# Kernel tuning notes

Measured on AMD Instinct MI355X. Metric: run time of the kernel, lower is better.

The kernel has to match this reference:

```python
import jax, jax.numpy as jnp
import numpy as np
from jax import lax

B = 512
MBD_B, MBD_C = 64, 16
FEAT = 40 * 4 * 4  # 640


def _conv(x, w, b):
    y = lax.conv_general_dilated(x, w, (1, 1), 'VALID',
                                 dimension_numbers=('NCHW', 'OIHW', 'NCHW'))
    return y + b[None, :, None, None]


def _maxpool2(x):
    return lax.reduce_window(x, -jnp.inf, lax.max,
                             (1, 1, 2, 2), (1, 1, 2, 2), 'VALID')


def setup_inputs() -> dict:
    key = jax.random.key(0)
    ks = jax.random.split(key, 10)
    def he(k, shape, fan_in):
        return jax.random.normal(k, shape, dtype=jnp.float32) * np.float32(1.0 / np.sqrt(fan_in))
    return {
        'x': jax.random.normal(ks[0], (B, 1, 28, 28), dtype=jnp.float32),
        'conv1_w': he(ks[1], (20, 1, 5, 5), 25),
        'conv1_b': jnp.zeros((20,), jnp.float32),
        'conv2_w': he(ks[2], (40, 20, 5, 5), 20 * 25),
        'conv2_b': jnp.zeros((40,), jnp.float32),
        'T': he(ks[3], (MBD_B * MBD_C, FEAT), FEAT),          # feature_scan_tensor (no bias)
        'fc1_w': he(ks[4], (100, FEAT + MBD_B), FEAT + MBD_B),
        'fc1_b': jnp.zeros((100,), jnp.float32),
        'fc2_w': he(ks[5], (1, 100), 100),
        'fc2_b': jnp.zeros((1,), jnp.float32),
    }


def reference(x, conv1_w, conv1_b, conv2_w, conv2_b, T, fc1_w, fc1_b, fc2_w, fc2_b):
    # conv feature extractor: [B,1,28,28] -> [B,40,4,4]
    h = _maxpool2(jax.nn.relu(_conv(x, conv1_w, conv1_b)))
    h = _maxpool2(jax.nn.relu(_conv(h, conv2_w, conv2_b)))
    feats = h.reshape(h.shape[0], -1)  # [B, 640]

    # minibatch discrimination: M = feats @ T^T -> [B, b, c]
    M = (feats @ T.T).reshape(-1, MBD_B, MBD_C)
    # pairwise L1 over c: [B, B, b] (includes j==i diagonal = 0, exp(0)=1, as in original)
    dist = jnp.abs(M[:, None, :, :] - M[None, :, :, :]).sum(axis=3)
    closeness = jnp.exp(-dist).sum(axis=1)  # [B, b]

    out = jnp.concatenate([feats, closeness], axis=1)  # [B, 640+b]
    out = jax.nn.relu(out @ fc1_w.T + fc1_b)
    # Dropout(p=0.2) omitted (deterministic eval-mode reference)
    out = jax.nn.sigmoid(out @ fc2_w.T + fc2_b)  # [B, 1]
    return out
```

## Files before the change

kernel.cpp:

```cpp
#include <hip/hip_runtime.h>


__global__ __launch_bounds__(256) void k0_wxform(const float* __restrict__ w,
                                                 float* __restrict__ ws) {
  const int e = blockIdx.x * 256 + threadIdx.x;
  if (e >= 32000) return;
  const int ocHalf = e / 16000;
  const int r = e - ocHalf * 16000;
  const int ic = r / 800;
  const int r2 = r - ic * 800;
  const int tap = r2 >> 5;
  const int slot = r2 & 31;
  const int q = slot & 7;
  const int grp = slot >> 3;
  float val = 0.f;
  if (q < 5) val = w[(ocHalf * 20 + grp * 5 + q) * 500 + ic * 25 + tap];
  ws[e] = val;
}

__global__ __launch_bounds__(128) void k1_conv1_pool(
    const float* __restrict__ x, const float* __restrict__ w,
    const float* __restrict__ bias, float* __restrict__ out) {
  __shared__ __align__(16) float img[784];
  __shared__ float wl[250];
  __shared__ float bl[10];
  const int imgId = blockIdx.x >> 1;
  const int half = blockIdx.x & 1;
  {
    const float4* src = reinterpret_cast<const float4*>(x + imgId * 784);
    float4* dst = reinterpret_cast<float4*>(img);
    for (int t = threadIdx.x; t < 196; t += 128) dst[t] = src[t];
  }
  for (int t = threadIdx.x; t < 250; t += 128) wl[t] = w[half * 250 + t];
  if (threadIdx.x < 10) bl[threadIdx.x] = bias[half * 10 + threadIdx.x];
  __syncthreads();

  for (int o = threadIdx.x; o < 1440; o += 128) {
    const int chl = o / 144;
    const int rem = o - chl * 144;
    const int py = rem / 12;
    const int px = rem - py * 12;
    const int oy = py * 2, ox = px * 2;
    float p[6][6];
    const float* ib = &img[oy * 28 + ox];
#pragma unroll
    for (int r = 0; r < 6; ++r) {
      const float2 v0 = *reinterpret_cast<const float2*>(&ib[r * 28 + 0]);
      const float2 v1 = *reinterpret_cast<const float2*>(&ib[r * 28 + 2]);
      const float2 v2 = *reinterpret_cast<const float2*>(&ib[r * 28 + 4]);
      p[r][0] = v0.x; p[r][1] = v0.y; p[r][2] = v1.x;
      p[r][3] = v1.y; p[r][4] = v2.x; p[r][5] = v2.y;
    }
    const float* wc = &wl[chl * 25];
    float s00 = 0.f, s01 = 0.f, s10 = 0.f, s11 = 0.f;
#pragma unroll
    for (int ky = 0; ky < 5; ++ky) {
#pragma unroll
      for (int kx = 0; kx < 5; ++kx) {
        const float ww = wc[ky * 5 + kx];
        s00 += p[ky][kx] * ww;
        s01 += p[ky][kx + 1] * ww;
        s10 += p[ky + 1][kx] * ww;
        s11 += p[ky + 1][kx + 1] * ww;
      }
    }
    const float m = fmaxf(fmaxf(s00, s01), fmaxf(s10, s11)) + bl[chl];
    out[imgId * 2880 + half * 1440 + o] = fmaxf(m, 0.f);
  }
}

__global__ __launch_bounds__(128) void k2_conv2_pool(
    const float* __restrict__ h1, const float* __restrict__ wsx,
    const float* __restrict__ bias, float* __restrict__ feats) {
  __shared__ __align__(16) float in[2880];
  __shared__ __align__(16) float wl[2][2][25][32];
  __shared__ float part[64][21];
  const int imgId = blockIdx.x >> 1;
  const int half = blockIdx.x & 1;
  const int tid = threadIdx.x;
  const int h = tid >> 6;
  const int grp = (tid >> 4) & 3;
  const int pos = tid & 15;
  const int py = pos >> 2, px = pos & 3;
  const int oy = py * 2, ox = px * 2;

  {
    const float4* src = reinterpret_cast<const float4*>(h1 + imgId * 2880);
    float4* dst = reinterpret_cast<float4*>(in);
    for (int t = tid; t < 720; t += 128) dst[t] = src[t];
  }
  const float4* wsrc = reinterpret_cast<const float4*>(wsx) + half * 4000;
  float4* wdst = reinterpret_cast<float4*>(wl);
  {
#pragma unroll
    for (int k = 0; k < 4; ++k) {
      const int e = tid + k * 128;
      if (e < 400) {
        const int hs = (e >= 200) ? 1 : 0;
        const int idx = e - hs * 200;
        wdst[hs * 400 + idx] = wsrc[(hs * 10 + 0) * 200 + idx];
      }
    }
  }
  __syncthreads();

  float acc[5][4];
#pragma unroll
  for (int q = 0; q < 5; ++q)
#pragma unroll
    for (int pp = 0; pp < 4; ++pp) acc[q][pp] = 0.f;

  for (int s = 0; s < 10; ++s) {
    const int p0 = s & 1;
    float4 sv[4];
    if (s < 9) {
#pragma unroll
      for (int k = 0; k < 4; ++k) {
        const int e = tid + k * 128;
        if (e < 400) {
          const int hs = (e >= 200) ? 1 : 0;
          const int idx = e - hs * 200;
          sv[k] = wsrc[(hs * 10 + s + 1) * 200 + idx];
        }
      }
    }
    const int myic = h * 10 + s;
    float p[6][6];
    {
      const float* ib = &in[myic * 144 + oy * 12 + ox];
#pragma unroll
      for (int r = 0; r < 6; ++r) {
        const float2 v0 = *reinterpret_cast<const float2*>(&ib[r * 12 + 0]);
        const float2 v1 = *reinterpret_cast<const float2*>(&ib[r * 12 + 2]);
        const float2 v2 = *reinterpret_cast<const float2*>(&ib[r * 12 + 4]);
        p[r][0] = v0.x; p[r][1] = v0.y; p[r][2] = v1.x;
        p[r][3] = v1.y; p[r][4] = v2.x; p[r][5] = v2.y;
      }
    }
#pragma unroll
    for (int ky = 0; ky < 5; ++ky) {
#pragma unroll
      for (int kx = 0; kx < 5; ++kx) {
        const int tap = ky * 5 + kx;
        const float4 w4 =
            *reinterpret_cast<const float4*>(&wl[h][p0][tap][grp * 8]);
        const float w4b = wl[h][p0][tap][grp * 8 + 4];
        const float i00 = p[ky][kx];
        const float i01 = p[ky][kx + 1];
        const float i10 = p[ky + 1][kx];
        const float i11 = p[ky + 1][kx + 1];
        acc[0][0] += i00 * w4.x; acc[0][1] += i01 * w4.x;
        acc[0][2] += i10 * w4.x; acc[0][3] += i11 * w4.x;
        acc[1][0] += i00 * w4.y; acc[1][1] += i01 * w4.y;
        acc[1][2] += i10 * w4.y; acc[1][3] += i11 * w4.y;
        acc[2][0] += i00 * w4.z; acc[2][1] += i01 * w4.z;
        acc[2][2] += i10 * w4.z; acc[2][3] += i11 * w4.z;
        acc[3][0] += i00 * w4.w; acc[3][1] += i01 * w4.w;
        acc[3][2] += i10 * w4.w; acc[3][3] += i11 * w4.w;
        acc[4][0] += i00 * w4b; acc[4][1] += i01 * w4b;
        acc[4][2] += i10 * w4b; acc[4][3] += i11 * w4b;
      }
    }
    if (s < 9) {
#pragma unroll
      for (int k = 0; k < 4; ++k) {
        const int e = tid + k * 128;
        if (e < 400) {
          const int hs = (e >= 200) ? 1 : 0;
          const int idx = e - hs * 200;
          wdst[hs * 400 + ((s + 1) & 1) * 200 + idx] = sv[k];
        }
      }
    }
    __syncthreads();
  }

  if (tid >= 64) {
    const int t2 = tid - 64;
#pragma unroll
    for (int q = 0; q < 5; ++q)
#pragma unroll
      for (int pp = 0; pp < 4; ++pp) part[t2][q * 4 + pp] = acc[q][pp];
  }
  __syncthreads();
  if (tid < 64) {
#pragma unroll
    for (int q = 0; q < 5; ++q) {
      const int ch = half * 20 + grp * 5 + q;
      const float a0 = acc[q][0] + part[tid][q * 4 + 0];
      const float a1 = acc[q][1] + part[tid][q * 4 + 1];
      const float a2 = acc[q][2] + part[tid][q * 4 + 2];
      const float a3 = acc[q][3] + part[tid][q * 4 + 3];
      const float m = fmaxf(fmaxf(a0, a1), fmaxf(a2, a3)) + bias[ch];
      feats[imgId * 640 + ch * 16 + pos] = fmaxf(m, 0.f);
    }
  }
}

__global__ __launch_bounds__(128) void k3_gemm(
    const float* __restrict__ A, const float* __restrict__ Bm,
    float* __restrict__ C) {
  __shared__ __align__(16) float As[16][36];
  __shared__ __align__(16) float Bs[16][36];
  const int tid = threadIdx.x;
  const int tx = tid & 15;
  const int ty = tid >> 4;
  const int i0 = blockIdx.y * 16;
  const int j0 = blockIdx.x * 32;
  float acc[2][2] = {{0.f, 0.f}, {0.f, 0.f}};

  for (int k0 = 0; k0 < 640; k0 += 16) {
    if (tid < 64) {
      const int m = tid >> 2, kq = tid & 3;
      const float4 av =
          *reinterpret_cast<const float4*>(A + (i0 + m) * 640 + k0 + kq * 4);
      As[kq * 4 + 0][m] = av.x;
      As[kq * 4 + 1][m] = av.y;
      As[kq * 4 + 2][m] = av.z;
      As[kq * 4 + 3][m] = av.w;
    }
    {
      const int n = tid >> 2, kq = tid & 3;
      const float4 bv =
          *reinterpret_cast<const float4*>(Bm + (j0 + n) * 640 + k0 + kq * 4);
      Bs[kq * 4 + 0][n] = bv.x;
      Bs[kq * 4 + 1][n] = bv.y;
      Bs[kq * 4 + 2][n] = bv.z;
      Bs[kq * 4 + 3][n] = bv.w;
    }
    __syncthreads();
#pragma unroll
    for (int kk = 0; kk < 16; ++kk) {
      const float2 a2 = *reinterpret_cast<const float2*>(&As[kk][ty * 2]);
      const float2 b2 = *reinterpret_cast<const float2*>(&Bs[kk][tx * 2]);
      acc[0][0] += a2.x * b2.x; acc[0][1] += a2.x * b2.y;
      acc[1][0] += a2.y * b2.x; acc[1][1] += a2.y * b2.y;
    }
    __syncthreads();
  }
#pragma unroll
  for (int u = 0; u < 2; ++u) {
    float2 st = make_float2(acc[u][0], acc[u][1]);
    *reinterpret_cast<float2*>(&C[(i0 + ty * 2 + u) * 1024 + j0 + tx * 2]) = st;
  }
}

__global__ __launch_bounds__(256) void k4_mbd(const float* __restrict__ M,
                                              float* __restrict__ cp) {
  __shared__ float4 jb4[2][4][256];
  const int bid = blockIdx.x;
  const int ig = bid >> 4;
  const int jq = bid & 15;
  const int t = threadIdx.x;
  const int b = t & 63;
  const int g = t >> 6;
  const int i0 = ig * 16 + g * 4;
  const float4* Mf4 = reinterpret_cast<const float4*>(M);

  float4 mi[4][4];
#pragma unroll
  for (int u = 0; u < 4; ++u) {
#pragma unroll
    for (int q = 0; q < 4; ++q) mi[u][q] = Mf4[(i0 + u) * 256 + b * 4 + q];
  }
  const int wslot = (t >> 2) * 4 + ((t & 3) ^ ((t >> 3) & 3));
  {
#pragma unroll
    for (int k = 0; k < 4; ++k)
      jb4[0][k][wslot] = Mf4[(jq * 32 + k) * 256 + t];
  }
  __syncthreads();

  float acc[4] = {0.f, 0.f, 0.f, 0.f};
  const int xr = (b >> 1) & 3;
  for (int c = 0; c < 8; ++c) {
    float4 st[4];
    if (c < 7) {
#pragma unroll
      for (int k = 0; k < 4; ++k)
        st[k] = Mf4[(jq * 32 + (c + 1) * 4 + k) * 256 + t];
    }
    const int cbuf = c & 1;
#pragma unroll
    for (int jj = 0; jj < 4; ++jj) {
      const float4* row = jb4[cbuf][jj];
      float4 mj[4];
#pragma unroll
      for (int q = 0; q < 4; ++q) mj[q] = row[b * 4 + (q ^ xr)];
#pragma unroll
      for (int u = 0; u < 4; ++u) {
        float dist =
            fabsf(mi[u][0].x - mj[0].x) + fabsf(mi[u][0].y - mj[0].y) +
            fabsf(mi[u][0].z - mj[0].z) + fabsf(mi[u][0].w - mj[0].w) +
            fabsf(mi[u][1].x - mj[1].x) + fabsf(mi[u][1].y - mj[1].y) +
            fabsf(mi[u][1].z - mj[1].z) + fabsf(mi[u][1].w - mj[1].w) +
            fabsf(mi[u][2].x - mj[2].x) + fabsf(mi[u][2].y - mj[2].y) +
            fabsf(mi[u][2].z - mj[2].z) + fabsf(mi[u][2].w - mj[2].w) +
            fabsf(mi[u][3].x - mj[3].x) + fabsf(mi[u][3].y - mj[3].y) +
            fabsf(mi[u][3].z - mj[3].z) + fabsf(mi[u][3].w - mj[3].w);
        acc[u] += __expf(-dist);
      }
    }
    if (c < 7) {
#pragma unroll
      for (int k = 0; k < 4; ++k) jb4[(c + 1) & 1][k][wslot] = st[k];
    }
    __syncthreads();
  }
#pragma unroll
  for (int u = 0; u < 4; ++u)
    cp[(jq * 512 + i0 + u) * 64 + b] = acc[u];
}

__global__ __launch_bounds__(256) void k5_head(
    const float* __restrict__ feats, const float* __restrict__ cp,
    const float* __restrict__ w1, const float* __restrict__ b1,
    const float* __restrict__ w2, const float* __restrict__ b2,
    float* __restrict__ out) {
  __shared__ __align__(16) float v[704];
  __shared__ float hb[100];
  const int i = blockIdx.x;
  const int tid = threadIdx.x;
  float4* v4 = reinterpret_cast<float4*>(v);
  if (tid < 160)
    v4[tid] = reinterpret_cast<const float4*>(feats + i * 640)[tid];
  if (tid >= 192) {
    const int bb = tid - 192;
    float s = 0.f;
#pragma unroll
    for (int q = 0; q < 16; ++q) s += cp[(q * 512 + i) * 64 + bb];
    v[640 + bb] = s;
  }
  __syncthreads();
  const int wave = tid >> 6;
  const int lane = tid & 63;
  for (int r = wave; r < 100; r += 4) {
    const float4* wr = reinterpret_cast<const float4*>(w1 + r * 704);
    const float4 wa = wr[lane];
    const float4 wb = wr[lane + 64];
    const float4 va = v4[lane];
    const float4 vb = v4[lane + 64];
    float s = wa.x * va.x + wa.y * va.y + wa.z * va.z + wa.w * va.w +
              wb.x * vb.x + wb.y * vb.y + wb.z * vb.z + wb.w * vb.w;
    if (lane < 48) {
      const float4 wc = wr[lane + 128];
      const float4 vc = v4[lane + 128];
      s += wc.x * vc.x + wc.y * vc.y + wc.z * vc.z + wc.w * vc.w;
    }
#pragma unroll
    for (int off = 32; off; off >>= 1) s += __shfl_xor(s, off);
    if (lane == 0) hb[r] = fmaxf(s + b1[r], 0.f) * w2[r];
  }
  __syncthreads();
  if (tid < 64) {
    float s = hb[tid] + ((tid < 36) ? hb[tid + 64] : 0.f);
#pragma unroll
    for (int off = 32; off; off >>= 1) s += __shfl_xor(s, off);
    if (tid == 0) out[i] = 1.f / (1.f + __expf(-(s + b2[0])));
  }
}

extern "C" void kernel_launch(void* const* d_in, const int* in_sizes, int n_in,
                              void* d_out, int out_size, void* d_ws,
                              size_t ws_size, hipStream_t stream) {
  const float* x   = (const float*)d_in[0];
  const float* c1w = (const float*)d_in[1];
  const float* c1b = (const float*)d_in[2];
  const float* c2w = (const float*)d_in[3];
  const float* c2b = (const float*)d_in[4];
  const float* T   = (const float*)d_in[5];
  const float* f1w = (const float*)d_in[6];
  const float* f1b = (const float*)d_in[7];
  const float* f2w = (const float*)d_in[8];
  const float* f2b = (const float*)d_in[9];
  float* out = (float*)d_out;

  float* h1     = (float*)d_ws;
  float* feats  = h1 + 512 * 2880;
  float* M      = feats + 512 * 640;
  float* wstage = M;
  float* cp     = h1;

  k0_wxform<<<125, 256, 0, stream>>>(c2w, wstage);
  k1_conv1_pool<<<1024, 128, 0, stream>>>(x, c1w, c1b, h1);
  k2_conv2_pool<<<1024, 128, 0, stream>>>(h1, wstage, c2b, feats);
  k3_gemm<<<dim3(32, 32), 128, 0, stream>>>(feats, T, M);
  k4_mbd<<<512, 256, 0, stream>>>(M, cp);
  k5_head<<<512, 256, 0, stream>>>(feats, cp, f1w, f1b, f2w, f2b, out);
}
```

Baseline: 195.4 us.

## Fuse conv stages into one kernel and use split-bf16 MFMA for the feature GEMM

Merges conv1+pool and conv2+pool into a single kernel that keeps the first-stage activations in shared memory, handling two images per block. This removes the global round-trip of the intermediate activations and one launch. It also replaces the scalar fp32 GEMM with an MFMA bf16 GEMM that splits each operand into high and low bf16 parts (three products) to approximate fp32 accuracy. The prep kernel now also converts T to hi/lo bf16 every call, which adds extra memory traffic and a small loss of precision in exchange.

```diff
diff --git a/kernel.cpp b/kernel.cpp
--- a/kernel.cpp
+++ b/kernel.cpp
@@ -1,247 +1,301 @@
 #include <hip/hip_runtime.h>
 
 
-__global__ __launch_bounds__(256) void k0_wxform(const float* __restrict__ w,
-                                                 float* __restrict__ ws) {
-  const int e = blockIdx.x * 256 + threadIdx.x;
-  if (e >= 32000) return;
-  const int ocHalf = e / 16000;
-  const int r = e - ocHalf * 16000;
-  const int ic = r / 800;
-  const int r2 = r - ic * 800;
-  const int tap = r2 >> 5;
-  const int slot = r2 & 31;
-  const int q = slot & 7;
-  const int grp = slot >> 3;
-  float val = 0.f;
-  if (q < 5) val = w[(ocHalf * 20 + grp * 5 + q) * 500 + ic * 25 + tap];
-  ws[e] = val;
-}
-
-__global__ __launch_bounds__(128) void k1_conv1_pool(
-    const float* __restrict__ x, const float* __restrict__ w,
-    const float* __restrict__ bias, float* __restrict__ out) {
-  __shared__ __align__(16) float img[784];
-  __shared__ float wl[250];
-  __shared__ float bl[10];
-  const int imgId = blockIdx.x >> 1;
-  const int half = blockIdx.x & 1;
+typedef __attribute__((ext_vector_type(8))) short bf16x8;
+typedef __attribute__((ext_vector_type(4))) float f32x4;
+
+static __device__ __forceinline__ unsigned short f2bf(float x) {
+  unsigned int u = __float_as_uint(x);
+  unsigned int r = (u + 0x7fffu + ((u >> 16) & 1u)) >> 16;
+  return (unsigned short)r;
+}
+static __device__ __forceinline__ float bf2f(unsigned short h) {
+  return __uint_as_float(((unsigned int)h) << 16);
+}
+
+__global__ __launch_bounds__(256) void kP_prep(
+    const float* __restrict__ c2w, const float* __restrict__ T,
+    float* __restrict__ ws2, unsigned short* __restrict__ Th,
+    unsigned short* __restrict__ Tl) {
+  const int idx = blockIdx.x * 256 + threadIdx.x;
+  if (idx < 655360) {
+    const float v = T[idx];
+    const unsigned short h = f2bf(v);
+    Th[idx] = h;
+    Tl[idx] = f2bf(v - bf2f(h));
+  }
+  if (idx < 32000) {
+    const int ic = idx / 1600;
+    const int r = idx - ic * 1600;
+    const int tap = r >> 6;
+    const int slot = r & 63;
+    const int grp = slot >> 3;
+    const int q = slot & 7;
+    float val = 0.f;
+    if (q < 5) val = c2w[(grp * 5 + q) * 500 + ic * 25 + tap];
+    ws2[idx] = val;
+  }
+}
+
+__global__ __launch_bounds__(256) void kC_conv(
+    const float* __restrict__ x, const float* __restrict__ c1w,
+    const float* __restrict__ c1b, const float* __restrict__ ws2,
+    const float* __restrict__ c2b, float* __restrict__ feats,
+    unsigned short* __restrict__ fh, unsigned short* __restrict__ fl) {
+  __shared__ __align__(16) float img[2][784];
+  __shared__ __align__(16) float h1s[2][2880];
+  __shared__ float wl1[500];
+  __shared__ float bl1[20];
+  __shared__ float bl2[40];
+  __shared__ __align__(16) float wl2[2][2][1600];
+  __shared__ float mg[2][64][41];
+
+  const int tid = threadIdx.x;
+  const int slot = tid >> 7;
+  const int lt = tid & 127;
+  const int imgId = blockIdx.x * 2 + slot;
+
   {
-    const float4* src = reinterpret_cast<const float4*>(x + imgId * 784);
-    float4* dst = reinterpret_cast<float4*>(img);
-    for (int t = threadIdx.x; t < 196; t += 128) dst[t] = src[t];
-  }
-  for (int t = threadIdx.x; t < 250; t += 128) wl[t] = w[half * 250 + t];
-  if (threadIdx.x < 10) bl[threadIdx.x] = bias[half * 10 + threadIdx.x];
-  __syncthreads();
-
-  for (int o = threadIdx.x; o < 1440; o += 128) {
-    const int chl = o / 144;
-    const int rem = o - chl * 144;
-    const int py = rem / 12;
-    const int px = rem - py * 12;
-    const int oy = py * 2, ox = px * 2;
-    float p[6][6];
-    const float* ib = &img[oy * 28 + ox];
+    float4* dst = reinterpret_cast<float4*>(&img[0][0]);
+    for (int t = tid; t < 392; t += 256) {
+      const int which = t / 196;
+      const int within = t - which * 196;
+      dst[t] = reinterpret_cast<const float4*>(
+          x + (blockIdx.x * 2 + which) * 784)[within];
+    }
+  }
+  for (int t = tid; t < 500; t += 256) wl1[t] = c1w[t];
+  if (tid < 20) bl1[tid] = c1b[tid];
+  if (tid >= 64 && tid < 104) bl2[tid - 64] = c2b[tid - 64];
+  __syncthreads();
+
+  for (int qd = lt; qd < 720; qd += 128) {
+    const int ch = qd / 36;
+    const int rem = qd - ch * 36;
+    const int py = rem / 3;
+    const int qx = rem - py * 3;
+    const int r0 = py * 2;
+    const int c0 = qx * 8;
+    float p[6][12];
 #pragma unroll
     for (int r = 0; r < 6; ++r) {
-      const float2 v0 = *reinterpret_cast<const float2*>(&ib[r * 28 + 0]);
-      const float2 v1 = *reinterpret_cast<const float2*>(&ib[r * 28 + 2]);
-      const float2 v2 = *reinterpret_cast<const float2*>(&ib[r * 28 + 4]);
-      p[r][0] = v0.x; p[r][1] = v0.y; p[r][2] = v1.x;
-      p[r][3] = v1.y; p[r][4] = v2.x; p[r][5] = v2.y;
-    }
-    const float* wc = &wl[chl * 25];
-    float s00 = 0.f, s01 = 0.f, s10 = 0.f, s11 = 0.f;
+      const float* ib = &img[slot][(r0 + r) * 28 + c0];
+      const float4 a = *reinterpret_cast<const float4*>(ib);
+      const float4 b = *reinterpret_cast<const float4*>(ib + 4);
+      const float4 c = *reinterpret_cast<const float4*>(ib + 8);
+      p[r][0] = a.x; p[r][1] = a.y; p[r][2] = a.z; p[r][3] = a.w;
+      p[r][4] = b.x; p[r][5] = b.y; p[r][6] = b.z; p[r][7] = b.w;
+      p[r][8] = c.x; p[r][9] = c.y; p[r][10] = c.z; p[r][11] = c.w;
+    }
+    float s[16];
+#pragma unroll
+    for (int u = 0; u < 16; ++u) s[u] = 0.f;
+    const float* wc = &wl1[ch * 25];
 #pragma unroll
     for (int ky = 0; ky < 5; ++ky) {
 #pragma unroll
       for (int kx = 0; kx < 5; ++kx) {
-        const float ww = wc[ky * 5 + kx];
-        s00 += p[ky][kx] * ww;
-        s01 += p[ky][kx + 1] * ww;
-        s10 += p[ky + 1][kx] * ww;
-        s11 += p[ky + 1][kx + 1] * ww;
-      }
-    }
-    const float m = fmaxf(fmaxf(s00, s01), fmaxf(s10, s11)) + bl[chl];
-    out[imgId * 2880 + half * 1440 + o] = fmaxf(m, 0.f);
-  }
-}
-
-__global__ __launch_bounds__(128) void k2_conv2_pool(
-    const float* __restrict__ h1, const float* __restrict__ wsx,
-    const float* __restrict__ bias, float* __restrict__ feats) {
-  __shared__ __align__(16) float in[2880];
-  __shared__ __align__(16) float wl[2][2][25][32];
-  __shared__ float part[64][21];
-  const int imgId = blockIdx.x >> 1;
-  const int half = blockIdx.x & 1;
-  const int tid = threadIdx.x;
-  const int h = tid >> 6;
-  const int grp = (tid >> 4) & 3;
-  const int pos = tid & 15;
-  const int py = pos >> 2, px = pos & 3;
-  const int oy = py * 2, ox = px * 2;
+        const float w = wc[ky * 5 + kx];
+#pragma unroll
+        for (int u = 0; u < 4; ++u) {
+#pragma unroll
+          for (int dy = 0; dy < 2; ++dy) {
+#pragma unroll
+            for (int dx = 0; dx < 2; ++dx) {
+              s[u * 4 + dy * 2 + dx] += p[ky + dy][2 * u + dx + kx] * w;
+            }
+          }
+        }
+      }
+    }
+    const float bb = bl1[ch];
+    float4 o;
+    o.x = fmaxf(fmaxf(fmaxf(s[0], s[1]), fmaxf(s[2], s[3])) + bb, 0.f);
+    o.y = fmaxf(fmaxf(fmaxf(s[4], s[5]), fmaxf(s[6], s[7])) + bb, 0.f);
+    o.z = fmaxf(fmaxf(fmaxf(s[8], s[9]), fmaxf(s[10], s[11])) + bb, 0.f);
+    o.w = fmaxf(fmaxf(fmaxf(s[12], s[13]), fmaxf(s[14], s[15])) + bb, 0.f);
+    *reinterpret_cast<float4*>(&h1s[slot][ch * 144 + py * 12 + qx * 4]) = o;
+  }
 
   {
-    const float4* src = reinterpret_cast<const float4*>(h1 + imgId * 2880);
-    float4* dst = reinterpret_cast<float4*>(in);
-    for (int t = tid; t < 720; t += 128) dst[t] = src[t];
-  }
-  const float4* wsrc = reinterpret_cast<const float4*>(wsx) + half * 4000;
-  float4* wdst = reinterpret_cast<float4*>(wl);
-  {
+    float4* wlf4 = reinterpret_cast<float4*>(&wl2[0][0][0]);
+    const float4* wsf4 = reinterpret_cast<const float4*>(ws2);
 #pragma unroll
     for (int k = 0; k < 4; ++k) {
-      const int e = tid + k * 128;
-      if (e < 400) {
-        const int hs = (e >= 200) ? 1 : 0;
-        const int idx = e - hs * 200;
-        wdst[hs * 400 + idx] = wsrc[(hs * 10 + 0) * 200 + idx];
-      }
-    }
-  }
-  __syncthreads();
-
-  float acc[5][4];
+      const int e = tid + k * 256;
+      if (e < 800) {
+        const int str = e / 400;
+        const int i4 = e - str * 400;
+        wlf4[(str * 2 + 0) * 400 + i4] = wsf4[(str * 10 + 0) * 400 + i4];
+      }
+    }
+  }
+  __syncthreads();
+
+  const int h = lt >> 6;
+  const int grp = (lt >> 3) & 7;
+  const int pp = lt & 7;
+  const int oy = (pp >> 1) * 2;
+  const int ox = (pp & 1) * 4;
+  float acc[5][8];
 #pragma unroll
   for (int q = 0; q < 5; ++q)
 #pragma unroll
-    for (int pp = 0; pp < 4; ++pp) acc[q][pp] = 0.f;
-
+    for (int u = 0; u < 8; ++u) acc[q][u] = 0.f;
+
+  float4* wlf4 = reinterpret_cast<float4*>(&wl2[0][0][0]);
+  const float4* wsf4 = reinterpret_cast<const float4*>(ws2);
   for (int s = 0; s < 10; ++s) {
     const int p0 = s & 1;
     float4 sv[4];
     if (s < 9) {
 #pragma unroll
       for (int k = 0; k < 4; ++k) {
-        const int e = tid + k * 128;
-        if (e < 400) {
-          const int hs = (e >= 200) ? 1 : 0;
-          const int idx = e - hs * 200;
-          sv[k] = wsrc[(hs * 10 + s + 1) * 200 + idx];
+        const int e = tid + k * 256;
+        if (e < 800) {
+          const int str = e / 400;
+          const int i4 = e - str * 400;
+          sv[k] = wsf4[(str * 10 + s + 1) * 400 + i4];
         }
       }
     }
-    const int myic = h * 10 + s;
-    float p[6][6];
-    {
-      const float* ib = &in[myic * 144 + oy * 12 + ox];
-#pragma unroll
-      for (int r = 0; r < 6; ++r) {
-        const float2 v0 = *reinterpret_cast<const float2*>(&ib[r * 12 + 0]);
-        const float2 v1 = *reinterpret_cast<const float2*>(&ib[r * 12 + 2]);
-        const float2 v2 = *reinterpret_cast<const float2*>(&ib[r * 12 + 4]);
-        p[r][0] = v0.x; p[r][1] = v0.y; p[r][2] = v1.x;
-        p[r][3] = v1.y; p[r][4] = v2.x; p[r][5] = v2.y;
-      }
-    }
+    const int ic = h * 10 + s;
+    float p[6][8];
+#pragma unroll
+    for (int r = 0; r < 6; ++r) {
+      const float* ib = &h1s[slot][ic * 144 + (oy + r) * 12 + ox];
+      const float4 a = *reinterpret_cast<const float4*>(ib);
+      const float4 b = *reinterpret_cast<const float4*>(ib + 4);
+      p[r][0] = a.x; p[r][1] = a.y; p[r][2] = a.z; p[r][3] = a.w;
+      p[r][4] = b.x; p[r][5] = b.y; p[r][6] = b.z; p[r][7] = b.w;
+    }
+    const float* wbase = &wl2[h][p0][0];
 #pragma unroll
     for (int ky = 0; ky < 5; ++ky) {
 #pragma unroll
       for (int kx = 0; kx < 5; ++kx) {
         const int tap = ky * 5 + kx;
         const float4 w4 =
-            *reinterpret_cast<const float4*>(&wl[h][p0][tap][grp * 8]);
-        const float w4b = wl[h][p0][tap][grp * 8 + 4];
-        const float i00 = p[ky][kx];
-        const float i01 = p[ky][kx + 1];
-        const float i10 = p[ky + 1][kx];
-        const float i11 = p[ky + 1][kx + 1];
-        acc[0][0] += i00 * w4.x; acc[0][1] += i01 * w4.x;
-        acc[0][2] += i10 * w4.x; acc[0][3] += i11 * w4.x;
-        acc[1][0] += i00 * w4.y; acc[1][1] += i01 * w4.y;
-        acc[1][2] += i10 * w4.y; acc[1][3] += i11 * w4.y;
-        acc[2][0] += i00 * w4.z; acc[2][1] += i01 * w4.z;
-        acc[2][2] += i10 * w4.z; acc[2][3] += i11 * w4.z;
-        acc[3][0] += i00 * w4.w; acc[3][1] += i01 * w4.w;
-        acc[3][2] += i10 * w4.w; acc[3][3] += i11 * w4.w;
-        acc[4][0] += i00 * w4b; acc[4][1] += i01 * w4b;
-        acc[4][2] += i10 * w4b; acc[4][3] += i11 * w4b;
+            *reinterpret_cast<const float4*>(&wbase[tap * 64 + grp * 8]);
+        const float w4b = wbase[tap * 64 + grp * 8 + 4];
+#pragma unroll
+        for (int pooled = 0; pooled < 2; ++pooled) {
+#pragma unroll
+          for (int dy = 0; dy < 2; ++dy) {
+#pragma unroll
+            for (int dx = 0; dx < 2; ++dx) {
+              const int u = pooled * 4 + dy * 2 + dx;
+              const float iv = p[ky + dy][pooled * 2 + dx + kx];
+              acc[0][u] += iv * w4.x;
+              acc[1][u] += iv * w4.y;
+              acc[2][u] += iv * w4.z;
+              acc[3][u] += iv * w4.w;
+              acc[4][u] += iv * w4b;
+            }
+          }
+        }
       }
     }
     if (s < 9) {
 #pragma unroll
       for (int k = 0; k < 4; ++k) {
-        const int e = tid + k * 128;
-        if (e < 400) {
-          const int hs = (e >= 200) ? 1 : 0;
-          const int idx = e - hs * 200;
-          wdst[hs * 400 + ((s + 1) & 1) * 200 + idx] = sv[k];
+        const int e = tid + k * 256;
+        if (e < 800) {
+          const int str = e / 400;
+          const int i4 = e - str * 400;
+          wlf4[(str * 2 + ((s + 1) & 1)) * 400 + i4] = sv[k];
         }
       }
     }
     __syncthreads();
   }
 
-  if (tid >= 64) {
-    const int t2 = tid - 64;
+  const int midx = (grp << 3) | pp;
+  if (h == 1) {
 #pragma unroll
     for (int q = 0; q < 5; ++q)
 #pragma unroll
-      for (int pp = 0; pp < 4; ++pp) part[t2][q * 4 + pp] = acc[q][pp];
-  }
-  __syncthreads();
-  if (tid < 64) {
+      for (int u = 0; u < 8; ++u) mg[slot][midx][q * 8 + u] = acc[q][u];
+  }
+  __syncthreads();
+  if (h == 0) {
+    const int pos0 = (pp >> 1) * 4 + (pp & 1) * 2;
 #pragma unroll
     for (int q = 0; q < 5; ++q) {
-      const int ch = half * 20 + grp * 5 + q;
-      const float a0 = acc[q][0] + part[tid][q * 4 + 0];
-      const float a1 = acc[q][1] + part[tid][q * 4 + 1];
-      const float a2 = acc[q][2] + part[tid][q * 4 + 2];
-      const float a3 = acc[q][3] + part[tid][q * 4 + 3];
-      const float m = fmaxf(fmaxf(a0, a1), fmaxf(a2, a3)) + bias[ch];
-      feats[imgId * 640 + ch * 16 + pos] = fmaxf(m, 0.f);
-    }
-  }
-}
-
-__global__ __launch_bounds__(128) void k3_gemm(
-    const float* __restrict__ A, const float* __restrict__ Bm,
-    float* __restrict__ C) {
-  __shared__ __align__(16) float As[16][36];
-  __shared__ __align__(16) float Bs[16][36];
+      const int ch = grp * 5 + q;
+      float a[8];
+#pragma unroll
+      for (int u = 0; u < 8; ++u) a[u] = acc[q][u] + mg[slot][midx][q * 8 + u];
+      const float bb = bl2[ch];
+      const float r0v =
+          fmaxf(fmaxf(fmaxf(a[0], a[1]), fmaxf(a[2], a[3])) + bb, 0.f);
+      const float r1v =
+          fmaxf(fmaxf(fmaxf(a[4], a[5]), fmaxf(a[6], a[7])) + bb, 0.f);
+      const int off = imgId * 640 + ch * 16 + pos0;
+      *reinterpret_cast<float2*>(&feats[off]) = make_float2(r0v, r1v);
+      const unsigned short h0 = f2bf(r0v), h1v = f2bf(r1v);
+      ushort2 hv; hv.x = h0; hv.y = h1v;
+      ushort2 lv;
+      lv.x = f2bf(r0v - bf2f(h0));
+      lv.y = f2bf(r1v - bf2f(h1v));
+      *reinterpret_cast<ushort2*>(&fh[off]) = hv;
+      *reinterpret_cast<ushort2*>(&fl[off]) = lv;
+    }
+  }
+}
+
+__global__ __launch_bounds__(256) void k3m_gemm(
+    const unsigned short* __restrict__ fh, const unsigned short* __restrict__ fl,
+    const unsigned short* __restrict__ Th, const unsigned short* __restrict__ Tl,
+    float* __restrict__ M) {
+  __shared__ short Ah[64][40];
+  __shared__ short Al[64][40];
+  __shared__ short Bh[64][40];
+  __shared__ short Bl[64][40];
   const int tid = threadIdx.x;
-  const int tx = tid & 15;
-  const int ty = tid >> 4;
-  const int i0 = blockIdx.y * 16;
-  const int j0 = blockIdx.x * 32;
-  float acc[2][2] = {{0.f, 0.f}, {0.f, 0.f}};
-
-  for (int k0 = 0; k0 < 640; k0 += 16) {
-    if (tid < 64) {
-      const int m = tid >> 2, kq = tid & 3;
-      const float4 av =
-          *reinterpret_cast<const float4*>(A + (i0 + m) * 640 + k0 + kq * 4);
-      As[kq * 4 + 0][m] = av.x;
-      As[kq * 4 + 1][m] = av.y;
-      As[kq * 4 + 2][m] = av.z;
-      As[kq * 4 + 3][m] = av.w;
-    }
-    {
-      const int n = tid >> 2, kq = tid & 3;
-      const float4 bv =
-          *reinterpret_cast<const float4*>(Bm + (j0 + n) * 640 + k0 + kq * 4);
-      Bs[kq * 4 + 0][n] = bv.x;
-      Bs[kq * 4 + 1][n] = bv.y;
-      Bs[kq * 4 + 2][n] = bv.z;
-      Bs[kq * 4 + 3][n] = bv.w;
-    }
+  const int i0 = blockIdx.y * 64;
+  const int j0 = blockIdx.x * 64;
+  const int row = tid >> 2, kq = tid & 3;
+  const int l = tid & 63, w = tid >> 6;
+  const int fr = l & 15, kslot = (l >> 4) * 8;
+
+  f32x4 acc[4];
+#pragma unroll
+  for (int js = 0; js < 4; ++js) acc[js] = (f32x4){0.f, 0.f, 0.f, 0.f};
+
+  for (int k0 = 0; k0 < 640; k0 += 32) {
+    const int ga = (i0 + row) * 640 + k0 + kq * 8;
+    const int gb = (j0 + row) * 640 + k0 + kq * 8;
+    const uint4 vah = *reinterpret_cast<const uint4*>(fh + ga);
+    const uint4 val_ = *reinterpret_cast<const uint4*>(fl + ga);
+    const uint4 vbh = *reinterpret_cast<const uint4*>(Th + gb);
+    const uint4 vbl = *reinterpret_cast<const uint4*>(Tl + gb);
     __syncthreads();
-#pragma unroll
-    for (int kk = 0; kk < 16; ++kk) {
-      const float2 a2 = *reinterpret_cast<const float2*>(&As[kk][ty * 2]);
-      const float2 b2 = *reinterpret_cast<const float2*>(&Bs[kk][tx * 2]);
-      acc[0][0] += a2.x * b2.x; acc[0][1] += a2.x * b2.y;
-      acc[1][0] += a2.y * b2.x; acc[1][1] += a2.y * b2.y;
-    }
+    *reinterpret_cast<uint4*>(&Ah[row][kq * 8]) = vah;
+    *reinterpret_cast<uint4*>(&Al[row][kq * 8]) = val_;
+    *reinterpret_cast<uint4*>(&Bh[row][kq * 8]) = vbh;
+    *reinterpret_cast<uint4*>(&Bl[row][kq * 8]) = vbl;
     __syncthreads();
-  }
-#pragma unroll
-  for (int u = 0; u < 2; ++u) {
-    float2 st = make_float2(acc[u][0], acc[u][1]);
-    *reinterpret_cast<float2*>(&C[(i0 + ty * 2 + u) * 1024 + j0 + tx * 2]) = st;
+    const bf16x8 aH = *reinterpret_cast<const bf16x8*>(&Ah[w * 16 + fr][kslot]);
+    const bf16x8 aL = *reinterpret_cast<const bf16x8*>(&Al[w * 16 + fr][kslot]);
+#pragma unroll
+    for (int js = 0; js < 4; ++js) {
+      const bf16x8 bH =
+          *reinterpret_cast<const bf16x8*>(&Bh[js * 16 + fr][kslot]);
+      const bf16x8 bL =
+          *reinterpret_cast<const bf16x8*>(&Bl[js * 16 + fr][kslot]);
+      acc[js] = __builtin_amdgcn_mfma_f32_16x16x32_bf16(aH, bH, acc[js], 0, 0, 0);
+      acc[js] = __builtin_amdgcn_mfma_f32_16x16x32_bf16(aL, bH, acc[js], 0, 0, 0);
+      acc[js] = __builtin_amdgcn_mfma_f32_16x16x32_bf16(aH, bL, acc[js], 0, 0, 0);
+    }
+  }
+#pragma unroll
+  for (int js = 0; js < 4; ++js) {
+#pragma unroll
+    for (int r = 0; r < 4; ++r) {
+      M[(i0 + w * 16 + (l >> 4) * 4 + r) * 1024 + j0 + js * 16 + (l & 15)] =
+          acc[js][r];
+    }
   }
 }
 
@@ -283,10 +337,10 @@
     const int cbuf = c & 1;
 #pragma unroll
     for (int jj = 0; jj < 4; ++jj) {
-      const float4* row = jb4[cbuf][jj];
+      const float4* rowp = jb4[cbuf][jj];
       float4 mj[4];
 #pragma unroll
-      for (int q = 0; q < 4; ++q) mj[q] = row[b * 4 + (q ^ xr)];
+      for (int q = 0; q < 4; ++q) mj[q] = rowp[b * 4 + (q ^ xr)];
 #pragma unroll
       for (int u = 0; u < 4; ++u) {
         float dist =
@@ -375,16 +429,18 @@
   const float* f2b = (const float*)d_in[9];
   float* out = (float*)d_out;
 
-  float* h1     = (float*)d_ws;
-  float* feats  = h1 + 512 * 2880;
-  float* M      = feats + 512 * 640;
-  float* wstage = M;
-  float* cp     = h1;
-
-  k0_wxform<<<125, 256, 0, stream>>>(c2w, wstage);
-  k1_conv1_pool<<<1024, 128, 0, stream>>>(x, c1w, c1b, h1);
-  k2_conv2_pool<<<1024, 128, 0, stream>>>(h1, wstage, c2b, feats);
-  k3_gemm<<<dim3(32, 32), 128, 0, stream>>>(feats, T, M);
+  float* feats = (float*)d_ws;
+  float* M     = feats + 327680;
+  float* cp    = M + 524288;
+  float* ws2   = cp + 524288;
+  unsigned short* fh = (unsigned short*)(ws2 + 32000);
+  unsigned short* fl = fh + 327680;
+  unsigned short* Th = fl + 327680;
+  unsigned short* Tl = Th + 655360;
+
+  kP_prep<<<2560, 256, 0, stream>>>(c2w, T, ws2, Th, Tl);
+  kC_conv<<<256, 256, 0, stream>>>(x, c1w, c1b, ws2, c2b, feats, fh, fl);
+  k3m_gemm<<<dim3(16, 8), 256, 0, stream>>>(fh, fl, Th, Tl, M);
   k4_mbd<<<512, 256, 0, stream>>>(M, cp);
   k5_head<<<512, 256, 0, stream>>>(feats, cp, f1w, f1b, f2w, f2b, out);
 }
```

Measured after the change: 175.8 us. 10.1% less time.
